# Kernel optimization log

Measured on AMD Instinct MI355X. Metric: run time of the kernel, lower is better.

## Reference

```python
import jax, jax.numpy as jnp
import numpy as np

GRID = 256          # grid_size
PAD = 30            # padding_size
GLOBAL = GRID + 2 * PAD   # 316
OUT = 512           # deform_input_size
K = 2 * PAD + 1     # 61 Gaussian kernel


def make_gaussian(size=K, a=1.0, b=0.5, fwhm1=100.0, fwhm2=25.0):
    x = np.arange(size, dtype=np.float64)
    c = size // 2
    r2 = (x[None, :] - c) ** 2 + (x[:, None] - c) ** 2
    g1 = np.exp(-4.0 * np.log(2.0) * r2 / fwhm1 ** 2)
    g2 = np.exp(-4.0 * np.log(2.0) * r2 / fwhm2 ** 2)
    return (a * g1 - b * g2).astype(np.float32)


def p_basis():
    # P[0,i,j] = (j - PAD)/(GRID-1) ; P[1,i,j] = (i - PAD)/(GRID-1)
    coord = (jnp.arange(GLOBAL, dtype=jnp.float32) - PAD) / (GRID - 1.0)
    px = jnp.broadcast_to(coord[None, :], (GLOBAL, GLOBAL))
    py = jnp.broadcast_to(coord[:, None], (GLOBAL, GLOBAL))
    return jnp.stack([px, py], axis=0)  # [2, 316, 316]


def base_grid():
    lin = jnp.linspace(-1.0, 1.0, OUT, dtype=jnp.float32)
    w = jnp.broadcast_to(lin[None, :], (OUT, OUT))  # x varies along columns
    h = jnp.broadcast_to(lin[:, None], (OUT, OUT))  # y varies along rows
    return jnp.stack([w, h], axis=-1)  # [512, 512, 2]


def grid_sample_bilinear(img, grid):
    """F.grid_sample, mode=bilinear, padding_mode=zeros, align_corners=True.
    img: [B,C,H,W], grid: [B,Hg,Wg,2] with (x,y) in [-1,1]."""
    B, C, H, W = img.shape
    gx = (grid[..., 0] + 1.0) * (W - 1) * 0.5
    gy = (grid[..., 1] + 1.0) * (H - 1) * 0.5
    x0 = jnp.floor(gx); y0 = jnp.floor(gy)
    wx1 = gx - x0; wx0 = 1.0 - wx1
    wy1 = gy - y0; wy0 = 1.0 - wy1

    def gather(ix, iy):
        valid = ((ix >= 0) & (ix <= W - 1) & (iy >= 0) & (iy <= H - 1)).astype(img.dtype)
        ixc = jnp.clip(ix, 0, W - 1).astype(jnp.int32)
        iyc = jnp.clip(iy, 0, H - 1).astype(jnp.int32)
        v = jax.vmap(lambda im, yy, xx: im[:, yy, xx])(img, iyc, ixc)  # [B,C,Hg,Wg]
        return v * valid[:, None]

    out = (gather(x0, y0) * (wx0 * wy0)[:, None]
           + gather(x0 + 1, y0) * (wx1 * wy0)[:, None]
           + gather(x0, y0 + 1) * (wx0 * wy1)[:, None]
           + gather(x0 + 1, y0 + 1) * (wx1 * wy1)[:, None])
    return out


def setup_inputs() -> dict:
    key = jax.random.key(0)
    k1, k2 = jax.random.split(key)
    x = jax.random.normal(k1, (8, 32, 512, 512), dtype=jnp.float32)
    xs = jax.random.uniform(k2, (8, 1, 256, 256), dtype=jnp.float32)
    gauss_kernel = jnp.asarray(make_gaussian())  # [61,61] fixed conv weight
    return {"x": x, "xs": xs, "gauss_kernel": gauss_kernel}


def reference(x, xs, gauss_kernel):
    B = xs.shape[0]
    xs = xs.reshape(B, 1, GRID, GRID)
    # ReplicationPad2d(PAD)
    xs_hm = jnp.pad(xs, ((0, 0), (0, 0), (PAD, PAD), (PAD, PAD)), mode="edge")  # [B,1,316,316]
    P = p_basis()  # [2,316,316]
    # channel 0: xs_hm (-> p_filter); channels 1,2: P * xs (-> x/y numerators)
    stacked = jnp.concatenate([xs_hm, P[None] * xs_hm], axis=1)  # [B,3,316,316]
    inp = stacked.reshape(B * 3, 1, GLOBAL, GLOBAL)
    kern = gauss_kernel.reshape(1, 1, K, K)
    conv = jax.lax.conv_general_dilated(inp, kern, (1, 1), "VALID")  # [B*3,1,256,256]
    conv = conv.reshape(B, 3, GRID, GRID)
    p_f = conv[:, 0]
    x_f = conv[:, 1] / p_f
    y_f = conv[:, 2] / p_f
    xg = jnp.clip(x_f * 2.0 - 1.0, -1.0, 1.0)
    yg = jnp.clip(y_f * 2.0 - 1.0, -1.0, 1.0)
    grid = jnp.stack([xg, yg], axis=1)  # [B,2,256,256]
    # nn.Upsample bilinear (align_corners=False) == jax.image.resize half-pixel bilinear
    grid_up = jax.image.resize(grid, (B, 2, OUT, OUT), method="bilinear")
    grid_l = jnp.transpose(grid_up, (0, 2, 3, 1))  # [B,512,512,2]
    grid_r = (49.0 * base_grid()[None] + grid_l) / 50.0
    x_sampled = grid_sample_bilinear(x, grid_r)  # [B,C,512,512]
    return x_sampled, grid_up
```

## Files before the change

kernel.cpp:

```cpp
#include <hip/hip_runtime.h>
#include <math.h>

#define GRID_N 256
#define PADN   30
#define GLOB_N 316
#define KS     61
#define OUT_N  512
#define BATCH  8
#define CHAN   32

#define TW     128
#define TH     8
#define SROWS  13
#define SCOLS  144
#define SC4    36
#define NSLOT  (SROWS * SC4)
#define TSZ    (SROWS * SCOLS)

typedef float v4f __attribute__((ext_vector_type(4)));

__device__ __forceinline__ void compute_weights(float* w1, float* w2) {
    int t = threadIdx.x;
    if (t < KS) {
        double d  = (double)(t - PADN);
        double r2 = d * d;
        const double c = 2.772588722239781;
        w1[t] = (float)exp(-c * r2 / 10000.0);
        w2[t] = (float)exp(-c * r2 / 625.0);
    }
}

__global__ __launch_bounds__(256) void hpass_kernel(const float* __restrict__ xs,
                                                    float* __restrict__ H) {
    __shared__ float srow[GLOB_N];
    __shared__ float w1[KS], w2[KS];
    int b  = blockIdx.x / GLOB_N;
    int gi = blockIdx.x % GLOB_N;
    int t  = threadIdx.x;

    compute_weights(w1, w2);

    int iy = gi - PADN;
    iy = iy < 0 ? 0 : (iy > GRID_N - 1 ? GRID_N - 1 : iy);
    const float* src = xs + ((size_t)b * GRID_N + iy) * GRID_N;
    for (int j = t; j < GLOB_N; j += 256) {
        int ix = j - PADN;
        ix = ix < 0 ? 0 : (ix > GRID_N - 1 ? GRID_N - 1 : ix);
        srow[j] = src[ix];
    }
    __syncthreads();

    float a1 = 0.f, a2 = 0.f, a3 = 0.f, a4 = 0.f;
    for (int v = 0; v < KS; ++v) {
        float s  = srow[t + v];
        float cc = (float)(t + v - PADN) * (1.0f / 255.0f);
        float cs = cc * s;
        float cw1 = w1[v], cw2 = w2[v];
        a1 += cw1 * s;
        a2 += cw2 * s;
        a3 += cw1 * cs;
        a4 += cw2 * cs;
    }
    size_t cst  = (size_t)GLOB_N * GRID_N;
    size_t base = ((size_t)(b * 4) * GLOB_N + gi) * GRID_N + t;
    H[base]           = a1;
    H[base + cst]     = a2;
    H[base + 2 * cst] = a3;
    H[base + 3 * cst] = a4;
}

__global__ __launch_bounds__(256) void vpass_kernel(const float* __restrict__ H,
                                                    float* __restrict__ g256) {
    __shared__ float w1[KS], w2[KS];
    int bid = (int)blockIdx.x;
    bid = (bid & 7) * 256 + (bid >> 3);
    int b = bid >> 8;
    int y = bid & 255;
    int t = threadIdx.x;

    compute_weights(w1, w2);
    __syncthreads();

    const float* Hb = H + (size_t)b * 4 * GLOB_N * GRID_N;
    size_t cst = (size_t)GLOB_N * GRID_N;

    float s1 = 0.f, s2 = 0.f, sx1 = 0.f, sx2 = 0.f, sy1 = 0.f, sy2 = 0.f;
    for (int u = 0; u < KS; ++u) {
        size_t off = (size_t)(y + u) * GRID_N + t;
        float h1 = Hb[off];
        float h2 = Hb[off + cst];
        float h3 = Hb[off + 2 * cst];
        float h4 = Hb[off + 3 * cst];
        float cw1 = w1[u], cw2 = w2[u];
        float cc = (float)(y + u - PADN) * (1.0f / 255.0f);
        s1  += cw1 * h1;
        s2  += cw2 * h2;
        sx1 += cw1 * h3;
        sx2 += cw2 * h4;
        sy1 += cw1 * (cc * h1);
        sy2 += cw2 * (cc * h2);
    }
    float p  = s1 - 0.5f * s2;
    float xf = (sx1 - 0.5f * sx2) / p;
    float yf = (sy1 - 0.5f * sy2) / p;
    float xg = fminf(fmaxf(xf * 2.0f - 1.0f, -1.0f), 1.0f);
    float yg = fminf(fmaxf(yf * 2.0f - 1.0f, -1.0f), 1.0f);

    size_t o = (size_t)(b * 2) * GRID_N * GRID_N + (size_t)y * GRID_N + t;
    g256[o] = xg;
    g256[o + (size_t)GRID_N * GRID_N] = yg;
}

__global__ __launch_bounds__(256) void upsample_kernel(const float* __restrict__ g256,
                                                       float* __restrict__ gup) {
    int idx = blockIdx.x * 256 + threadIdx.x;
    int ox = idx & (OUT_N - 1);
    int oy = (idx >> 9) & (OUT_N - 1);
    int b  = idx >> 18;

    float sx = 0.5f * (float)ox - 0.25f;
    float sy = 0.5f * (float)oy - 0.25f;
    float fxf = floorf(sx), fyf = floorf(sy);
    int x0 = (int)fxf, y0 = (int)fyf;
    float fx = sx - fxf, fy = sy - fyf;
    int x0c = x0 < 0 ? 0 : x0;
    int x1c = x0 + 1 > GRID_N - 1 ? GRID_N - 1 : x0 + 1;
    int y0c = y0 < 0 ? 0 : y0;
    int y1c = y0 + 1 > GRID_N - 1 ? GRID_N - 1 : y0 + 1;

    for (int c = 0; c < 2; ++c) {
        const float* g = g256 + ((size_t)(b * 2 + c)) * GRID_N * GRID_N;
        float v00 = g[y0c * GRID_N + x0c];
        float v10 = g[y0c * GRID_N + x1c];
        float v01 = g[y1c * GRID_N + x0c];
        float v11 = g[y1c * GRID_N + x1c];
        float v = (v00 * (1.f - fx) + v10 * fx) * (1.f - fy)
                + (v01 * (1.f - fx) + v11 * fx) * fy;
        gup[((size_t)(b * 2 + c)) * OUT_N * OUT_N + (size_t)oy * OUT_N + ox] = v;
    }
}

template <int FUSED>
__global__ __launch_bounds__(256) void sample_kernel(const float* __restrict__ x,
                                                     const float* __restrict__ g256,
                                                     const float* __restrict__ gup_in,
                                                     float* __restrict__ gup_out,
                                                     float* __restrict__ out) {
    __shared__ float tile[2 * TSZ];

    int bid = (int)blockIdx.x;
    bid = (bid & 7) * 256 + (bid >> 3);
    int b  = bid >> 8;
    int tb = bid & 255;
    int tx = (tb & 3) * TW;
    int ty = (tb >> 2) * TH;

    int t   = threadIdx.x;
    int col = t & (TW - 1);
    int kk  = t >> 7;

    int row_base = ty - 2;
    int col_base = tx - 8;

    int off0 = 0, off1 = 0;
    {
        int k = t;
        int r = k / SC4, i = k - r * SC4;
        int rg = row_base + r; rg = rg < 0 ? 0 : (rg > OUT_N - 1 ? OUT_N - 1 : rg);
        int cg = col_base + i * 4; cg = cg < 0 ? 0 : (cg > OUT_N - 4 ? OUT_N - 4 : cg);
        off0 = rg * OUT_N + cg;
        k = t + 256;
        if (k < NSLOT) {
            r = k / SC4; i = k - r * SC4;
            rg = row_base + r; rg = rg < 0 ? 0 : (rg > OUT_N - 1 ? OUT_N - 1 : rg);
            cg = col_base + i * 4; cg = cg < 0 ? 0 : (cg > OUT_N - 4 ? OUT_N - 4 : cg);
            off1 = rg * OUT_N + cg;
        }
    }
    bool has1 = (t + 256) < NSLOT;

    float w00[4], w10[4], w01[4], w11[4];
    int lbase[4];
    {
        int ox = tx + col;
        float bx = -1.0f + (float)ox * (2.0f / 511.0f);

        float usx = 0.5f * (float)ox - 0.25f;
        float ufxf = floorf(usx);
        int ux0 = (int)ufxf;
        float ufx = usx - ufxf;
        int ux0c = ux0 < 0 ? 0 : ux0;
        int ux1c = ux0 + 1 > GRID_N - 1 ? GRID_N - 1 : ux0 + 1;
        const float* g0 = g256 + (size_t)(b * 2) * GRID_N * GRID_N;
        const float* g1 = g0 + GRID_N * GRID_N;
        size_t gplane = (size_t)OUT_N * OUT_N;

        #pragma unroll
        for (int j = 0; j < 4; ++j) {
            int oy = ty + kk + 2 * j;
            float gxu, gyu;
            if (FUSED) {
                float usy = 0.5f * (float)oy - 0.25f;
                float ufyf = floorf(usy);
                int uy0 = (int)ufyf;
                float ufy = usy - ufyf;
                int uy0c = uy0 < 0 ? 0 : uy0;
                int uy1c = uy0 + 1 > GRID_N - 1 ? GRID_N - 1 : uy0 + 1;
                {
                    float v00 = g0[uy0c * GRID_N + ux0c];
                    float v10 = g0[uy0c * GRID_N + ux1c];
                    float v01 = g0[uy1c * GRID_N + ux0c];
                    float v11 = g0[uy1c * GRID_N + ux1c];
                    gxu = (v00 * (1.f - ufx) + v10 * ufx) * (1.f - ufy)
                        + (v01 * (1.f - ufx) + v11 * ufx) * ufy;
                }
                {
                    float v00 = g1[uy0c * GRID_N + ux0c];
                    float v10 = g1[uy0c * GRID_N + ux1c];
                    float v01 = g1[uy1c * GRID_N + ux0c];
                    float v11 = g1[uy1c * GRID_N + ux1c];
                    gyu = (v00 * (1.f - ufx) + v10 * ufx) * (1.f - ufy)
                        + (v01 * (1.f - ufx) + v11 * ufx) * ufy;
                }
                size_t gidx = (size_t)(b * 2) * gplane + (size_t)oy * OUT_N + ox;
                __builtin_nontemporal_store(gxu, gup_out + gidx);
                __builtin_nontemporal_store(gyu, gup_out + gidx + gplane);
            } else {
                size_t gidx = (size_t)(b * 2) * gplane + (size_t)oy * OUT_N + ox;
                gxu = gup_in[gidx];
                gyu = gup_in[gidx + gplane];
            }

            float by = -1.0f + (float)oy * (2.0f / 511.0f);
            float gx = (49.0f * bx + gxu) * 0.02f;
            float gy = (49.0f * by + gyu) * 0.02f;
            float pxf = (gx + 1.0f) * 255.5f;
            float pyf = (gy + 1.0f) * 255.5f;
            float fx0 = floorf(pxf), fy0 = floorf(pyf);
            int x0 = (int)fx0, y0 = (int)fy0;
            float fx = pxf - fx0, fy = pyf - fy0;
            w00[j] = (1.f - fx) * (1.f - fy);
            w10[j] = fx * (1.f - fy);
            w01[j] = (1.f - fx) * fy;
            w11[j] = fx * fy;
            lbase[j] = (y0 - row_base) * SCOLS + (x0 - col_base);
        }
    }

    size_t plane = (size_t)OUT_N * OUT_N;
    const float* xb = x + (size_t)b * CHAN * plane;
    float* ob = out + (size_t)b * CHAN * plane;
    int ocol = tx + col;

    v4f pfA0 = *(const v4f*)(xb + off0);
    v4f pfA1 = has1 ? *(const v4f*)(xb + off1) : pfA0;
    v4f pfB0 = *(const v4f*)(xb + plane + off0);
    v4f pfB1 = has1 ? *(const v4f*)(xb + plane + off1) : pfB0;

    for (int c = 0; c < CHAN; ++c) {
        float* tb_ = tile + (c & 1) * TSZ;
        __syncthreads();
        *(v4f*)(tb_ + t * 4) = pfA0;
        if (has1) *(v4f*)(tb_ + (t + 256) * 4) = pfA1;
        pfA0 = pfB0; pfA1 = pfB1;
        if (c + 2 < CHAN) {
            const float* xc = xb + (size_t)(c + 2) * plane;
            pfB0 = *(const v4f*)(xc + off0);
            if (has1) pfB1 = *(const v4f*)(xc + off1);
        }
        __syncthreads();

        float* oc = ob + (size_t)c * plane;
        #pragma unroll
        for (int j = 0; j < 4; ++j) {
            int lb = lbase[j];
            float v00 = tb_[lb];
            float v10 = tb_[lb + 1];
            float v01 = tb_[lb + SCOLS];
            float v11 = tb_[lb + SCOLS + 1];
            float v = w00[j] * v00 + w10[j] * v10 + w01[j] * v01 + w11[j] * v11;
            int oy = ty + kk + 2 * j;
            __builtin_nontemporal_store(v, oc + (size_t)oy * OUT_N + ocol);
        }
    }
}

extern "C" void kernel_launch(void* const* d_in, const int* in_sizes, int n_in,
                              void* d_out, int out_size, void* d_ws, size_t ws_size,
                              hipStream_t stream) {
    (void)in_sizes; (void)n_in; (void)out_size;
    const float* x  = (const float*)d_in[0];
    const float* xs = (const float*)d_in[1];

    float* out = (float*)d_out;
    const size_t XS_OUT = (size_t)BATCH * CHAN * OUT_N * OUT_N;
    float* gup = out + XS_OUT;

    float* H = out;
    const size_t G256_BYTES = (size_t)BATCH * 2 * GRID_N * GRID_N * sizeof(float);
    bool fused = ws_size >= G256_BYTES;
    float* g256 = fused ? (float*)d_ws : out + 4u * 1024 * 1024;

    hipLaunchKernelGGL(hpass_kernel, dim3(BATCH * GLOB_N), dim3(256), 0, stream, xs, H);
    hipLaunchKernelGGL(vpass_kernel, dim3(BATCH * GRID_N), dim3(256), 0, stream, H, g256);
    if (fused) {
        hipLaunchKernelGGL((sample_kernel<1>), dim3(BATCH * OUT_N * OUT_N / (TW * TH)),
                           dim3(256), 0, stream, x, g256, gup, gup, out);
    } else {
        hipLaunchKernelGGL(upsample_kernel, dim3(BATCH * OUT_N * OUT_N / 256), dim3(256), 0,
                           stream, g256, gup);
        hipLaunchKernelGGL((sample_kernel<0>), dim3(BATCH * OUT_N * OUT_N / (TW * TH)),
                           dim3(256), 0, stream, x, g256, gup, gup, out);
    }
}
```

Measured before the change: 149.0 us.

## Stage sample tiles via direct global-to-LDS loads with manual vmcnt pipelining

Replaces the register-staged double buffer in the sampling kernel with global_load_lds DMA-style 16-byte loads straight into shared memory, synchronised by explicit s_waitcnt vmcnt counts and raw barriers. The halo tile shrinks (12 rows, 136 cols) so it fits the fixed lane-to-LDS layout of the load-to-LDS instruction. This removes the VGPR round trip and the LDS store instructions per channel. In exchange it relies on hand-counted outstanding memory ops interleaved with the nontemporal stores, and the halo margin is tighter, which risks wrong results if sample coordinates fall outside the smaller tile.

After: 151.9 us. Within noise of the previous version (+1.9%).

```diff
diff --git a/kernel.cpp b/kernel.cpp
--- a/kernel.cpp
+++ b/kernel.cpp
@@ -11,13 +11,19 @@
 
 #define TW     128
 #define TH     8
-#define SROWS  13
-#define SCOLS  144
-#define SC4    36
+#define SROWS  12
+#define SCOLS  136
+#define SC4    34
 #define NSLOT  (SROWS * SC4)
-#define TSZ    (SROWS * SCOLS)
+#define NSLOTPAD 512
+#define BUF_FLOATS (NSLOTPAD * 4)
 
 typedef float v4f __attribute__((ext_vector_type(4)));
+
+#define GLD16(gaddr, laddr)                                                       \
+    __builtin_amdgcn_global_load_lds(                                             \
+        (const __attribute__((address_space(1))) void*)(gaddr),                   \
+        (__attribute__((address_space(3))) void*)(laddr), 16, 0, 0)
 
 __device__ __forceinline__ void compute_weights(float* w1, float* w2) {
     int t = threadIdx.x;
@@ -146,7 +152,7 @@
                                                      const float* __restrict__ gup_in,
                                                      float* __restrict__ gup_out,
                                                      float* __restrict__ out) {
-    __shared__ float tile[2 * TSZ];
+    __shared__ float tile[2 * BUF_FLOATS];
 
     int bid = (int)blockIdx.x;
     bid = (bid & 7) * 256 + (bid >> 3);
@@ -160,24 +166,25 @@
     int kk  = t >> 7;
 
     int row_base = ty - 2;
-    int col_base = tx - 8;
-
-    int off0 = 0, off1 = 0;
+    int col_base = tx - 4;
+
+    int offA, offB;
     {
         int k = t;
         int r = k / SC4, i = k - r * SC4;
         int rg = row_base + r; rg = rg < 0 ? 0 : (rg > OUT_N - 1 ? OUT_N - 1 : rg);
         int cg = col_base + i * 4; cg = cg < 0 ? 0 : (cg > OUT_N - 4 ? OUT_N - 4 : cg);
-        off0 = rg * OUT_N + cg;
+        offA = rg * OUT_N + cg;
+        offB = offA;
         k = t + 256;
         if (k < NSLOT) {
             r = k / SC4; i = k - r * SC4;
             rg = row_base + r; rg = rg < 0 ? 0 : (rg > OUT_N - 1 ? OUT_N - 1 : rg);
             cg = col_base + i * 4; cg = cg < 0 ? 0 : (cg > OUT_N - 4 ? OUT_N - 4 : cg);
-            off1 = rg * OUT_N + cg;
+            offB = rg * OUT_N + cg;
         }
     }
-    bool has1 = (t + 256) < NSLOT;
+    int wbase = (t & ~63) * 4;
 
     float w00[4], w10[4], w01[4], w11[4];
     int lbase[4];
@@ -252,25 +259,25 @@
     float* ob = out + (size_t)b * CHAN * plane;
     int ocol = tx + col;
 
-    v4f pfA0 = *(const v4f*)(xb + off0);
-    v4f pfA1 = has1 ? *(const v4f*)(xb + off1) : pfA0;
-    v4f pfB0 = *(const v4f*)(xb + plane + off0);
-    v4f pfB1 = has1 ? *(const v4f*)(xb + plane + off1) : pfB0;
-
+    #define STAGE(c, bufIdx)                                                     \
+        do {                                                                     \
+            const float* xc_ = xb + (size_t)(c) * plane;                         \
+            GLD16(xc_ + offA, &tile[(bufIdx) * BUF_FLOATS + wbase]);             \
+            GLD16(xc_ + offB, &tile[(bufIdx) * BUF_FLOATS + 1024 + wbase]);      \
+        } while (0)
+
+    STAGE(0, 0);
+    STAGE(1, 1);
+
+    float v[4];
     for (int c = 0; c < CHAN; ++c) {
-        float* tb_ = tile + (c & 1) * TSZ;
-        __syncthreads();
-        *(v4f*)(tb_ + t * 4) = pfA0;
-        if (has1) *(v4f*)(tb_ + (t + 256) * 4) = pfA1;
-        pfA0 = pfB0; pfA1 = pfB1;
-        if (c + 2 < CHAN) {
-            const float* xc = xb + (size_t)(c + 2) * plane;
-            pfB0 = *(const v4f*)(xc + off0);
-            if (has1) pfB1 = *(const v4f*)(xc + off1);
-        }
-        __syncthreads();
-
-        float* oc = ob + (size_t)c * plane;
+        if (c == 0)            asm volatile("s_waitcnt vmcnt(2)" ::: "memory");
+        else if (c == CHAN - 1) asm volatile("s_waitcnt vmcnt(4)" ::: "memory");
+        else                    asm volatile("s_waitcnt vmcnt(6)" ::: "memory");
+        __builtin_amdgcn_s_barrier();
+        __builtin_amdgcn_sched_barrier(0);
+
+        const float* tb_ = &tile[(c & 1) * BUF_FLOATS];
         #pragma unroll
         for (int j = 0; j < 4; ++j) {
             int lb = lbase[j];
@@ -278,11 +285,23 @@
             float v10 = tb_[lb + 1];
             float v01 = tb_[lb + SCOLS];
             float v11 = tb_[lb + SCOLS + 1];
-            float v = w00[j] * v00 + w10[j] * v10 + w01[j] * v01 + w11[j] * v11;
+            v[j] = w00[j] * v00 + w10[j] * v10 + w01[j] * v01 + w11[j] * v11;
+        }
+
+        __builtin_amdgcn_sched_barrier(0);
+        __builtin_amdgcn_s_barrier();
+        __builtin_amdgcn_sched_barrier(0);
+
+        if (c + 2 < CHAN) STAGE(c + 2, c & 1);
+
+        float* oc = ob + (size_t)c * plane;
+        #pragma unroll
+        for (int j = 0; j < 4; ++j) {
             int oy = ty + kk + 2 * j;
-            __builtin_nontemporal_store(v, oc + (size_t)oy * OUT_N + ocol);
+            __builtin_nontemporal_store(v[j], oc + (size_t)oy * OUT_N + ocol);
         }
     }
+    #undef STAGE
 }
 
 extern "C" void kernel_launch(void* const* d_in, const int* in_sizes, int n_in,
```
